# Optimization experiments

Hardware: AMD Instinct MI355X
Metric: run time of the kernel (lower is better)

The kernel has to match this reference:

```python
import jax, jax.numpy as jnp
import numpy as np

B, G, D = 256, 64, 20          # batch, genes per term, subsystem output dim
T3, T2, T1, T0 = 2048, 512, 128, 1  # terms per stratum, deepest first
FAN = 4                        # children per internal term (root gets all T1)
EPS = 1e-5                     # BatchNorm1d eps


def setup_inputs() -> dict:
    key = jax.random.key(0)
    ks = jax.random.split(key, 32)
    def genes(k, T):
        # binary gene perturbation states (column 3 of go_gene_strata_state)
        return (jax.random.uniform(k, (B, T, G)) < 0.5).astype(jnp.float32)
    def lin(kw, kb, T, din):
        # nn.init.uniform_(w, -0.001, 0.001) per DCellSubsystem
        W = jax.random.uniform(kw, (T, din, D), minval=-0.001, maxval=0.001)
        b = jax.random.uniform(kb, (T, D), minval=-0.001, maxval=0.001)
        return W, b
    in3, in2, in1, in0 = G, FAN * D + G, FAN * D + G, T1 * D + G
    W3, b3 = lin(ks[0], ks[1], T3, in3)
    W2, b2 = lin(ks[2], ks[3], T2, in2)
    W1, b1 = lin(ks[4], ks[5], T1, in1)
    W0, b0 = lin(ks[6], ks[7], T0, in0)
    ones = lambda T: jnp.ones((T, D), jnp.float32)
    zeros = lambda T: jnp.zeros((T, D), jnp.float32)
    hw0 = jax.random.normal(ks[8], (T0, D, 1)) * 0.1
    hb0 = jnp.zeros((T0, 1), jnp.float32)
    return {
        'genes3': genes(ks[9], T3), 'genes2': genes(ks[10], T2),
        'genes1': genes(ks[11], T1), 'genes0': genes(ks[12], T0),
        'W3': W3, 'b3': b3, 'g3': ones(T3), 'be3': zeros(T3),
        'W2': W2, 'b2': b2, 'g2': ones(T2), 'be2': zeros(T2),
        'W1': W1, 'b1': b1, 'g1': ones(T1), 'be1': zeros(T1),
        'W0': W0, 'b0': b0, 'g0': ones(T0), 'be0': zeros(T0),
        'hw0': hw0, 'hb0': hb0,
    }


def _subsystem(x, W, b, g, be):
    # Linear -> BatchNorm1d (training mode, batch stats over axis 0) -> Tanh
    z = jnp.einsum('bti,tio->bto', x, W) + b          # [B, T, D]
    mu = jnp.mean(z, axis=0)
    var = jnp.var(z, axis=0)                           # biased, as in torch BN
    zn = (z - mu) * jax.lax.rsqrt(var + EPS)
    return jnp.tanh(zn * g + be)


def reference(genes3, genes2, genes1, genes0,
              W3, b3, g3, be3, W2, b2, g2, be2,
              W1, b1, g1, be1, W0, b0, g0, be0, hw0, hb0):
    # stratum 3 (leaves): input is gene states only
    h3 = _subsystem(genes3, W3, b3, g3, be3)           # [B, T3, D]
    # stratum 2: concat FAN contiguous children + own gene states
    x2 = jnp.concatenate([h3.reshape(B, T2, FAN * D), genes2], axis=-1)
    h2 = _subsystem(x2, W2, b2, g2, be2)               # [B, T2, D]
    x1 = jnp.concatenate([h2.reshape(B, T1, FAN * D), genes1], axis=-1)
    h1 = _subsystem(x1, W1, b1, g1, be1)               # [B, T1, D]
    # root: all T1 children + root gene states
    x0 = jnp.concatenate([h1.reshape(B, T0, T1 * D), genes0], axis=-1)
    h0 = _subsystem(x0, W0, b0, g0, be0)               # [B, 1, D]
    pred = jnp.einsum('bto,toc->btc', h0, hw0) + hb0   # root linear head
    return pred.reshape(B, 1)
```

## Files before the change

### kernel.cpp

```cpp
#include <hip/hip_runtime.h>
#include <hip/hip_fp16.h>


#define DEV static __device__ __forceinline__

constexpr int B_  = 256, G_ = 64, D_ = 20;
constexpr int T3_ = 2048, T2_ = 512, T1_ = 128;
constexpr float EPS_ = 1e-5f;

typedef unsigned char u8;
typedef unsigned long long u64;

constexpr size_t OFF_GTB3 = 0;
constexpr size_t SZ_GTB3 = (size_t)T3_ * B_ * 8;
constexpr size_t OFF_GTB2 = OFF_GTB3 + SZ_GTB3;
constexpr size_t SZ_GTB2 = (size_t)T2_ * B_ * 8;
constexpr size_t OFF_GTB1 = OFF_GTB2 + SZ_GTB2;
constexpr size_t SZ_GTB1 = (size_t)T1_ * B_ * 8;
constexpr size_t OFF_H2B = OFF_GTB1 + SZ_GTB1;
constexpr size_t SZ_H2 = (size_t)T2_ * B_ * D_ * 2;
constexpr size_t OFF_H1B = OFF_H2B + SZ_H2;
constexpr size_t SZ_H1 = (size_t)T1_ * B_ * D_ * 2;
constexpr size_t OFF_Z0B = OFF_H1B + SZ_H1;

typedef _Float16 half8_t __attribute__((ext_vector_type(8)));
typedef float f32x4 __attribute__((ext_vector_type(4)));

DEV half8_t as_h8(uint4 u) {
    union { uint4 u4; half8_t h; } c; c.u4 = u; return c.h;
}

DEV half8_t bits8_to_h8(uint byte) {
    uint4 r;
    r.x = ((byte & 1u)        | ((byte & 2u)   << 15)) * 0x3C00u;
    r.y = (((byte >> 2) & 1u) | ((byte & 8u)   << 13)) * 0x3C00u;
    r.z = (((byte >> 4) & 1u) | ((byte & 32u)  << 11)) * 0x3C00u;
    r.w = (((byte >> 6) & 1u) | ((byte & 128u) << 9))  * 0x3C00u;
    return as_h8(r);
}

DEV float fast_tanh(float x) {
    float e = __expf(2.0f * x);
    return fmaf(-2.0f, __builtin_amdgcn_rcpf(e + 1.0f), 1.0f);
}

__global__ __launch_bounds__(256, 8) void k_pack_all(
        const float* __restrict__ g3s, const float* __restrict__ g2s,
        const float* __restrict__ g1s,
        u64* __restrict__ d3, u64* __restrict__ d2, u64* __restrict__ d1) {
    constexpr int R3 = B_ * T3_;
    constexpr int R2 = B_ * T2_;
    const int lane = threadIdx.x & 63;
    int R0 = (blockIdx.x * 4 + (threadIdx.x >> 6)) * 8;
    const float* src; u64* dst; int shift;
    if (R0 < R3)            { src = g3s; dst = d3; shift = 11; }
    else if (R0 < R3 + R2)  { R0 -= R3; src = g2s; dst = d2; shift = 9; }
    else                    { R0 -= R3 + R2; src = g1s; dst = d1; shift = 7; }

    const float* p = src + (size_t)R0 * G_ + lane;
    float x[8];
#pragma unroll
    for (int r = 0; r < 8; ++r) x[r] = p[r * G_];
    u64 m[8];
#pragma unroll
    for (int r = 0; r < 8; ++r) m[r] = __ballot(x[r] != 0.0f);

    if (lane < 8) {
        u64 v = m[0];
        v = lane == 1 ? m[1] : v;
        v = lane == 2 ? m[2] : v;
        v = lane == 3 ? m[3] : v;
        v = lane == 4 ? m[4] : v;
        v = lane == 5 ? m[5] : v;
        v = lane == 6 ? m[6] : v;
        v = lane == 7 ? m[7] : v;
        const int R = R0 + lane;
        const int b = R >> shift, t = R - (b << shift);
        dst[(size_t)t * B_ + b] = v;
    }
}

__global__ __launch_bounds__(256, 2) void k_gemm32(
        const u64* __restrict__ gTb3, const u64* __restrict__ gTb2,
        const float* __restrict__ W3, const float* __restrict__ g3,
        const float* __restrict__ be3,
        const float* __restrict__ W2, const float* __restrict__ g2,
        const float* __restrict__ be2, __half* __restrict__ h2out) {
    constexpr int STRB3 = 72, STRB2 = 200;
    __shared__ __align__(16) __half h3loc[4 * B_ * D_ + 16];
    __shared__ __align__(16) __half WT3[2][32 * STRB3];
    __shared__ __align__(16) __half WT2[32 * STRB2];
    __shared__ u64 gmask[5][B_];
    __shared__ float sredb[2][4][16], qredb[2][4][16];
    __shared__ float gv3[4 * D_], bev3[4 * D_], gv2[D_], bev2[D_];

    const int t = blockIdx.x, tid = threadIdx.x;
    const int w = tid >> 6, lane = tid & 63;

    u64 mreg[5];
#pragma unroll
    for (int c = 0; c < 4; ++c)
        mreg[c] = gTb3[(size_t)(4 * t + c) * B_ + tid];
    mreg[4] = gTb2[(size_t)t * B_ + tid];

    {
        uint* WTu = (uint*)WT2;
        for (int j = tid; j < 32 * STRB2 / 2; j += 256) WTu[j] = 0;
        if (tid < 16) h3loc[4 * B_ * D_ + tid] = __half(0.0f);
    }
#pragma unroll
    for (int s = 0; s < 5; ++s) gmask[s][tid] = mreg[s];
    __syncthreads();

    if (tid < 4 * D_) {
        gv3[tid] = g3[(size_t)(4 * t) * D_ + tid];
        bev3[tid] = be3[(size_t)(4 * t) * D_ + tid];
    } else if (tid < 5 * D_) {
        gv2[tid - 4 * D_] = g2[(size_t)t * D_ + (tid - 4 * D_)];
        bev2[tid - 4 * D_] = be2[(size_t)t * D_ + (tid - 4 * D_)];
    }
    {
        constexpr int NW2 = (144 * D_ + 255) / 256;
        const float* Wt = W2 + (size_t)t * (144 * D_);
        float wst[NW2];
#pragma unroll
        for (int i = 0; i < NW2; ++i) {
            int j = tid + i * 256;
            wst[i] = (j < 144 * D_) ? Wt[j] : 0.0f;
        }
        const float* W3t = W3 + (size_t)(4 * t) * (G_ * D_);
        float w3st[5];
#pragma unroll
        for (int i = 0; i < 5; ++i) w3st[i] = W3t[tid + i * 256];
#pragma unroll
        for (int i = 0; i < NW2; ++i) {
            int j = tid + i * 256;
            if (j < 144 * D_) {
                int k_orig = j / D_, o = j - k_orig * D_;
                int k_lds;
                if (k_orig < 4 * D_) {
                    int c = k_orig / D_;
                    k_lds = c * 32 + (k_orig - c * D_);
                } else {
                    k_lds = 4 * 32 + (k_orig - 4 * D_);
                }
                WT2[o * STRB2 + k_lds] = __float2half(wst[i]);
            }
        }
#pragma unroll
        for (int i = 0; i < 5; ++i) {
            int j = tid + i * 256;
            int k = j / D_, o = j - k * D_;
            WT3[0][o * STRB3 + k] = __float2half(w3st[i]);
        }
    }
    __syncthreads();

    const int quad = lane >> 4, l15 = lane & 15;
    const int nt = w >> 1, mhalf = w & 1;
    const int ocol = nt * 16 + l15;
    const int brow_base = mhalf * 128;
    const int shq = quad * 8;
    const int oc = ocol < D_ ? ocol : D_ - 1;

#pragma unroll
    for (int c = 0; c < 4; ++c) {
        float wreg[5];
        if (c < 3) {
            const float* W3n = W3 + (size_t)(4 * t + c + 1) * (G_ * D_);
#pragma unroll
            for (int i = 0; i < 5; ++i) wreg[i] = W3n[tid + i * 256];
        }
        const __half* WTc = WT3[c & 1];
        half8_t Bf0 = as_h8(*(const uint4*)(WTc + ocol * STRB3 + quad * 8));
        half8_t Bf1 = as_h8(*(const uint4*)(WTc + ocol * STRB3 + 32 + quad * 8));

        f32x4 acc[8];
#pragma unroll
        for (int mt = 0; mt < 8; ++mt) acc[mt] = (f32x4){0.f, 0.f, 0.f, 0.f};
#pragma unroll
        for (int mt = 0; mt < 8; ++mt) {
            const int bA = brow_base + mt * 16 + l15;
            const u64 gm = gmask[c][bA];
            acc[mt] = __builtin_amdgcn_mfma_f32_16x16x32_f16(
                bits8_to_h8(((uint)gm >> shq) & 0xFFu), Bf0, acc[mt], 0, 0, 0);
            acc[mt] = __builtin_amdgcn_mfma_f32_16x16x32_f16(
                bits8_to_h8(((uint)(gm >> 32) >> shq) & 0xFFu), Bf1, acc[mt], 0, 0, 0);
        }

        if (c < 3) {
#pragma unroll
            for (int i = 0; i < 5; ++i) {
                int j = tid + i * 256;
                int k = j / D_, o = j - k * D_;
                WT3[(c + 1) & 1][o * STRB3 + k] = __float2half(wreg[i]);
            }
        }

        float s = 0.f, q = 0.f;
#pragma unroll
        for (int mt = 0; mt < 8; ++mt)
#pragma unroll
            for (int r = 0; r < 4; ++r) {
                float z = acc[mt][r];
                s += z; q += z * z;
            }
        s += __shfl_xor(s, 16, 64); q += __shfl_xor(q, 16, 64);
        s += __shfl_xor(s, 32, 64); q += __shfl_xor(q, 32, 64);
        if (lane < 16) { sredb[c & 1][w][lane] = s; qredb[c & 1][w][lane] = q; }
        __syncthreads();
        const float S = sredb[c & 1][2 * nt][l15] + sredb[c & 1][2 * nt + 1][l15];
        const float Q = qredb[c & 1][2 * nt][l15] + qredb[c & 1][2 * nt + 1][l15];
        const float mu  = S * (1.0f / B_);
        const float var = fmaxf(Q * (1.0f / B_) - mu * mu, 0.0f);
        const float rstd = rsqrtf(var + EPS_);
        const float A = rstd * gv3[c * D_ + oc];
        const float C = bev3[c * D_ + oc] - mu * A;
        if (ocol < D_) {
#pragma unroll
            for (int mt = 0; mt < 8; ++mt)
#pragma unroll
                for (int r = 0; r < 4; ++r) {
                    float h = fast_tanh(fmaf(A, acc[mt][r], C));
                    int b = brow_base + mt * 16 + quad * 4 + r;
                    h3loc[(size_t)(c * B_ + b) * D_ + ocol] = __float2half(h);
                }
        }
    }
    __syncthreads();

    half8_t Bf[6];
#pragma unroll
    for (int ks = 0; ks < 6; ++ks)
        Bf[ks] = as_h8(*(const uint4*)(WT2 + ocol * STRB2 + ks * 32 + quad * 8));

    f32x4 acc[8];
#pragma unroll
    for (int mt = 0; mt < 8; ++mt) acc[mt] = (f32x4){0.f, 0.f, 0.f, 0.f};
#pragma unroll
    for (int mt = 0; mt < 8; ++mt) {
        const int bA = brow_base + mt * 16 + l15;
        const u64 gm = gmask[4][bA];
#pragma unroll
        for (int c = 0; c < 4; ++c) {
            const __half* ap = h3loc + (size_t)(c * B_ + bA) * D_ + quad * 8;
            uint2 u0 = *(const uint2*)(ap);
            uint2 u1 = *(const uint2*)(ap + 4);
            acc[mt] = __builtin_amdgcn_mfma_f32_16x16x32_f16(
                as_h8(make_uint4(u0.x, u0.y, u1.x, u1.y)), Bf[c], acc[mt], 0, 0, 0);
        }
        acc[mt] = __builtin_amdgcn_mfma_f32_16x16x32_f16(
            bits8_to_h8(((uint)gm >> shq) & 0xFFu), Bf[4], acc[mt], 0, 0, 0);
        acc[mt] = __builtin_amdgcn_mfma_f32_16x16x32_f16(
            bits8_to_h8(((uint)(gm >> 32) >> shq) & 0xFFu), Bf[5], acc[mt], 0, 0, 0);
    }

    float s = 0.f, q = 0.f;
#pragma unroll
    for (int mt = 0; mt < 8; ++mt)
#pragma unroll
        for (int r = 0; r < 4; ++r) {
            float z = acc[mt][r];
            s += z; q += z * z;
        }
    s += __shfl_xor(s, 16, 64); q += __shfl_xor(q, 16, 64);
    s += __shfl_xor(s, 32, 64); q += __shfl_xor(q, 32, 64);
    if (lane < 16) { sredb[0][w][lane] = s; qredb[0][w][lane] = q; }
    __syncthreads();
    const float S = sredb[0][2 * nt][l15] + sredb[0][2 * nt + 1][l15];
    const float Q = qredb[0][2 * nt][l15] + qredb[0][2 * nt + 1][l15];
    const float mu  = S * (1.0f / B_);
    const float var = fmaxf(Q * (1.0f / B_) - mu * mu, 0.0f);
    const float rstd = rsqrtf(var + EPS_);
    const float A = rstd * gv2[oc];
    const float C = bev2[oc] - mu * A;

    __half* ebuf = WT2;
    if (ocol < D_) {
#pragma unroll
        for (int mt = 0; mt < 8; ++mt)
#pragma unroll
            for (int r = 0; r < 4; ++r) {
                float h = fast_tanh(fmaf(A, acc[mt][r], C));
                int b = brow_base + mt * 16 + quad * 4 + r;
                ebuf[b * D_ + ocol] = __float2half(h);
            }
    }
    __syncthreads();
    const uint4* src4 = (const uint4*)ebuf;
    uint4* dst4 = (uint4*)(h2out + (size_t)t * (B_ * D_));
    for (int j = tid; j < (B_ * D_) / 8; j += 256) dst4[j] = src4[j];
}

template <int T, int NCHILD>
__global__ __launch_bounds__(256, 4) void k_gemm(const __half* __restrict__ hsrc,
                                                 const u64* __restrict__ gTb,
                                                 const float* __restrict__ W,
                                                 const float* __restrict__ g,
                                                 const float* __restrict__ be,
                                                 __half* __restrict__ hout) {
    constexpr int K_IN = NCHILD * 20 + 64;
    constexpr int NK = NCHILD + 2;
    constexpr int STRB = NCHILD ? 200 : 72;
    constexpr int LDSH = (32 * STRB > B_ * D_) ? 32 * STRB : B_ * D_;
    __shared__ __align__(16) __half WT[LDSH];
    __shared__ float gv[D_], bev[D_];
    __shared__ float sred[4][16], qred[4][16];
    __shared__ u64 gmask[B_];

    const int t = blockIdx.x, tid = threadIdx.x;
    const int w = tid >> 6, lane = tid & 63;

    const u64 mreg = gTb[(size_t)t * B_ + tid];

    if (NCHILD) {
        uint* WTu = (uint*)WT;
        for (int j = tid; j < 32 * STRB / 2; j += 256) WTu[j] = 0;
    }
    gmask[tid] = mreg;
    __syncthreads();

    if (tid < D_) { gv[tid] = g[t * D_ + tid]; bev[tid] = be[t * D_ + tid]; }
    {
        constexpr int NST = (K_IN * D_ + 255) / 256;
        const float* Wt = W + (size_t)t * (K_IN * D_);
        float wst[NST];
#pragma unroll
        for (int i = 0; i < NST; ++i) {
            int j = tid + i * 256;
            wst[i] = (j < K_IN * D_) ? Wt[j] : 0.0f;
        }
#pragma unroll
        for (int i = 0; i < NST; ++i) {
            int j = tid + i * 256;
            if (j < K_IN * D_) {
                int k_orig = j / D_, o = j - k_orig * D_;
                int k_lds;
                if (NCHILD && k_orig < NCHILD * D_) {
                    int c = k_orig / D_;
                    k_lds = c * 32 + (k_orig - c * D_);
                } else {
                    k_lds = NCHILD * 32 + (k_orig - NCHILD * D_);
                }
                WT[o * STRB + k_lds] = __float2half(wst[i]);
            }
        }
    }
    __syncthreads();

    const int quad = lane >> 4, l15 = lane & 15;
    const int nt = w >> 1, mhalf = w & 1;
    const int ocol = nt * 16 + l15;
    const int brow_base = mhalf * 128;
    const int shq = quad * 8;

    half8_t Bf[NK];
#pragma unroll
    for (int ks = 0; ks < NK; ++ks)
        Bf[ks] = as_h8(*(const uint4*)(WT + ocol * STRB + ks * 32 + quad * 8));

    f32x4 acc[8];
#pragma unroll
    for (int mt = 0; mt < 8; ++mt) acc[mt] = (f32x4){0.f, 0.f, 0.f, 0.f};

#pragma unroll
    for (int mt = 0; mt < 8; ++mt) {
        const int bA = brow_base + mt * 16 + l15;
        const u64 gm = gmask[bA];
#pragma unroll
        for (int c = 0; c < NCHILD; ++c) {
            const __half* ap = hsrc + ((size_t)(NCHILD * t + c) * B_ + bA) * D_ + quad * 8;
            uint2 u0 = *(const uint2*)(ap);
            uint2 u1 = *(const uint2*)(ap + 4);
            acc[mt] = __builtin_amdgcn_mfma_f32_16x16x32_f16(
                as_h8(make_uint4(u0.x, u0.y, u1.x, u1.y)), Bf[c], acc[mt], 0, 0, 0);
        }
        acc[mt] = __builtin_amdgcn_mfma_f32_16x16x32_f16(
            bits8_to_h8(((uint)gm >> shq) & 0xFFu), Bf[NCHILD], acc[mt], 0, 0, 0);
        acc[mt] = __builtin_amdgcn_mfma_f32_16x16x32_f16(
            bits8_to_h8(((uint)(gm >> 32) >> shq) & 0xFFu), Bf[NCHILD + 1], acc[mt], 0, 0, 0);
    }

    float s = 0.f, q = 0.f;
#pragma unroll
    for (int mt = 0; mt < 8; ++mt)
#pragma unroll
        for (int r = 0; r < 4; ++r) {
            float z = acc[mt][r];
            s += z; q += z * z;
        }
    s += __shfl_xor(s, 16, 64); q += __shfl_xor(q, 16, 64);
    s += __shfl_xor(s, 32, 64); q += __shfl_xor(q, 32, 64);
    if (lane < 16) { sred[w][lane] = s; qred[w][lane] = q; }
    __syncthreads();
    const float S = sred[2 * nt][l15] + sred[2 * nt + 1][l15];
    const float Q = qred[2 * nt][l15] + qred[2 * nt + 1][l15];
    const float mu  = S * (1.0f / B_);
    const float var = fmaxf(Q * (1.0f / B_) - mu * mu, 0.0f);
    const float rstd = rsqrtf(var + EPS_);
    const int oc = ocol < D_ ? ocol : D_ - 1;
    const float A = rstd * gv[oc];
    const float C = bev[oc] - mu * A;

    if (ocol < D_) {
#pragma unroll
        for (int mt = 0; mt < 8; ++mt)
#pragma unroll
            for (int r = 0; r < 4; ++r) {
                float h = fast_tanh(fmaf(A, acc[mt][r], C));
                int b = brow_base + mt * 16 + quad * 4 + r;
                WT[b * D_ + ocol] = __float2half(h);
            }
    }
    __syncthreads();
    const uint4* src4 = (const uint4*)WT;
    uint4* dst4 = (uint4*)(hout + (size_t)t * (B_ * D_));
    for (int j = tid; j < (B_ * D_) / 8; j += 256) dst4[j] = src4[j];
}

__global__ __launch_bounds__(256, 4) void k_stage0a(const __half* __restrict__ h1,
                                                    const float* __restrict__ genes0,
                                                    const float* __restrict__ W0,
                                                    float* __restrict__ z0p) {
    const int b = blockIdx.x >> 2, s = blockIdx.x & 3, tid = threadIdx.x;
    const int kbase = 640 * s;
    float acc[D_] = {};
#pragma unroll
    for (int j = 0; j < 3; ++j) {
        int kl = tid + 256 * j;
        if (kl < 640) {
            int k = kbase + kl;
            int tt = k / D_, o = k - tt * D_;
            float xk = __half2float(h1[((size_t)tt * B_ + b) * D_ + o]);
            const float4* w = (const float4*)(W0 + (size_t)k * D_);
#pragma unroll
            for (int v = 0; v < D_ / 4; ++v) {
                float4 f = w[v];
                acc[4 * v + 0] = fmaf(xk, f.x, acc[4 * v + 0]);
                acc[4 * v + 1] = fmaf(xk, f.y, acc[4 * v + 1]);
                acc[4 * v + 2] = fmaf(xk, f.z, acc[4 * v + 2]);
                acc[4 * v + 3] = fmaf(xk, f.w, acc[4 * v + 3]);
            }
        }
    }
    if (s == 3 && tid < G_) {
        float xk = genes0[(size_t)b * G_ + tid];
        const float4* w = (const float4*)(W0 + (size_t)(T1_ * D_ + tid) * D_);
#pragma unroll
        for (int v = 0; v < D_ / 4; ++v) {
            float4 f = w[v];
            acc[4 * v + 0] = fmaf(xk, f.x, acc[4 * v + 0]);
            acc[4 * v + 1] = fmaf(xk, f.y, acc[4 * v + 1]);
            acc[4 * v + 2] = fmaf(xk, f.z, acc[4 * v + 2]);
            acc[4 * v + 3] = fmaf(xk, f.w, acc[4 * v + 3]);
        }
    }
    __shared__ float sred[4][D_];
    const int lane = tid & 63, wave = tid >> 6;
#pragma unroll
    for (int off = 32; off; off >>= 1)
#pragma unroll
        for (int o = 0; o < D_; ++o) acc[o] += __shfl_xor(acc[o], off, 64);
    if (lane == 0)
#pragma unroll
        for (int o = 0; o < D_; ++o) sred[wave][o] = acc[o];
    __syncthreads();
    if (tid < D_)
        z0p[((size_t)b * 4 + s) * D_ + tid] =
            sred[0][tid] + sred[1][tid] + sred[2][tid] + sred[3][tid];
}

__global__ __launch_bounds__(256) void k_stage0b(const float* __restrict__ z0p,
                                                 const float* __restrict__ g0,
                                                 const float* __restrict__ be0,
                                                 const float* __restrict__ hw0,
                                                 const float* __restrict__ hb0,
                                                 float* __restrict__ out) {
    const int tid = threadIdx.x;
    float acc[D_] = {};
#pragma unroll
    for (int s = 0; s < 4; ++s) {
        const float4* zp = (const float4*)(z0p + ((size_t)tid * 4 + s) * D_);
#pragma unroll
        for (int v = 0; v < D_ / 4; ++v) {
            float4 f = zp[v];
            acc[4 * v + 0] += f.x; acc[4 * v + 1] += f.y;
            acc[4 * v + 2] += f.z; acc[4 * v + 3] += f.w;
        }
    }
    __shared__ float sred[4][D_], qred[4][D_], Avec[D_], Cvec[D_], hwv[D_ + 1];
    const int lane = tid & 63, wave = tid >> 6;
    float s[D_], q[D_];
#pragma unroll
    for (int o = 0; o < D_; ++o) { s[o] = acc[o]; q[o] = acc[o] * acc[o]; }
#pragma unroll
    for (int off = 32; off; off >>= 1) {
#pragma unroll
        for (int o = 0; o < D_; ++o) {
            s[o] += __shfl_xor(s[o], off, 64);
            q[o] += __shfl_xor(q[o], off, 64);
        }
    }
    if (lane == 0) {
#pragma unroll
        for (int o = 0; o < D_; ++o) { sred[wave][o] = s[o]; qred[wave][o] = q[o]; }
    }
    __syncthreads();
    if (tid < D_) {
        float S = sred[0][tid] + sred[1][tid] + sred[2][tid] + sred[3][tid];
        float Q = qred[0][tid] + qred[1][tid] + qred[2][tid] + qred[3][tid];
        float mu  = S * (1.0f / B_);
        float var = fmaxf(Q * (1.0f / B_) - mu * mu, 0.0f);
        float rstd = rsqrtf(var + EPS_);
        float A = rstd * g0[tid];
        Avec[tid] = A;
        Cvec[tid] = be0[tid] - mu * A;
        hwv[tid] = hw0[tid];
    }
    if (tid == 0) hwv[D_] = hb0[0];
    __syncthreads();
    float pred = hwv[D_];
#pragma unroll
    for (int o = 0; o < D_; ++o) {
        float h = fast_tanh(fmaf(acc[o], Avec[o], Cvec[o]));
        pred = fmaf(h, hwv[o], pred);
    }
    out[tid] = pred;
}

extern "C" void kernel_launch(void* const* d_in, const int* in_sizes, int n_in,
                              void* d_out, int out_size, void* d_ws, size_t ws_size,
                              hipStream_t stream) {
    const float* genes3 = (const float*)d_in[0];
    const float* genes2 = (const float*)d_in[1];
    const float* genes1 = (const float*)d_in[2];
    const float* genes0 = (const float*)d_in[3];
    const float* W3  = (const float*)d_in[4];
    const float* g3  = (const float*)d_in[6];
    const float* be3 = (const float*)d_in[7];
    const float* W2  = (const float*)d_in[8];
    const float* g2  = (const float*)d_in[10];
    const float* be2 = (const float*)d_in[11];
    const float* W1  = (const float*)d_in[12];
    const float* g1  = (const float*)d_in[14];
    const float* be1 = (const float*)d_in[15];
    const float* W0  = (const float*)d_in[16];
    const float* g0  = (const float*)d_in[18];
    const float* be0 = (const float*)d_in[19];
    const float* hw0 = (const float*)d_in[20];
    const float* hb0 = (const float*)d_in[21];

    char* wsb = (char*)d_ws;
    u64* gTb3 = (u64*)(wsb + OFF_GTB3);
    u64* gTb2 = (u64*)(wsb + OFF_GTB2);
    u64* gTb1 = (u64*)(wsb + OFF_GTB1);
    __half* h2  = (__half*)(wsb + OFF_H2B);
    __half* h1  = (__half*)(wsb + OFF_H1B);
    float*  z0p = (float*)(wsb + OFF_Z0B);

    k_pack_all<<<688128 / 32, 256, 0, stream>>>(genes3, genes2, genes1,
                                                gTb3, gTb2, gTb1);
    k_gemm32<<<T2_, 256, 0, stream>>>(gTb3, gTb2, W3, g3, be3,
                                      W2, g2, be2, h2);
    k_gemm<T1_, 4><<<T1_, 256, 0, stream>>>(h2, gTb1, W1, g1, be1, h1);
    k_stage0a<<<B_ * 4, 256, 0, stream>>>(h1, genes0, W0, z0p);
    k_stage0b<<<1, 256, 0, stream>>>(z0p, g0, be0, hw0, hb0, (float*)d_out);
}
```

Baseline: 305.1 us.

## Fuse gene bit-packing into stratum-3/2 GEMM via cooperative grid sync

```diff
diff --git a/kernel.cpp b/kernel.cpp
--- a/kernel.cpp
+++ b/kernel.cpp
@@ -1,6 +1,9 @@
 #include <hip/hip_runtime.h>
 #include <hip/hip_fp16.h>
-
+#include <hip/hip_cooperative_groups.h>
+
+
+namespace cg = cooperative_groups;
 
 #define DEV static __device__ __forceinline__
 
@@ -44,44 +47,10 @@
     return fmaf(-2.0f, __builtin_amdgcn_rcpf(e + 1.0f), 1.0f);
 }
 
-__global__ __launch_bounds__(256, 8) void k_pack_all(
-        const float* __restrict__ g3s, const float* __restrict__ g2s,
-        const float* __restrict__ g1s,
-        u64* __restrict__ d3, u64* __restrict__ d2, u64* __restrict__ d1) {
-    constexpr int R3 = B_ * T3_;
-    constexpr int R2 = B_ * T2_;
-    const int lane = threadIdx.x & 63;
-    int R0 = (blockIdx.x * 4 + (threadIdx.x >> 6)) * 8;
-    const float* src; u64* dst; int shift;
-    if (R0 < R3)            { src = g3s; dst = d3; shift = 11; }
-    else if (R0 < R3 + R2)  { R0 -= R3; src = g2s; dst = d2; shift = 9; }
-    else                    { R0 -= R3 + R2; src = g1s; dst = d1; shift = 7; }
-
-    const float* p = src + (size_t)R0 * G_ + lane;
-    float x[8];
-#pragma unroll
-    for (int r = 0; r < 8; ++r) x[r] = p[r * G_];
-    u64 m[8];
-#pragma unroll
-    for (int r = 0; r < 8; ++r) m[r] = __ballot(x[r] != 0.0f);
-
-    if (lane < 8) {
-        u64 v = m[0];
-        v = lane == 1 ? m[1] : v;
-        v = lane == 2 ? m[2] : v;
-        v = lane == 3 ? m[3] : v;
-        v = lane == 4 ? m[4] : v;
-        v = lane == 5 ? m[5] : v;
-        v = lane == 6 ? m[6] : v;
-        v = lane == 7 ? m[7] : v;
-        const int R = R0 + lane;
-        const int b = R >> shift, t = R - (b << shift);
-        dst[(size_t)t * B_ + b] = v;
-    }
-}
-
-__global__ __launch_bounds__(256, 2) void k_gemm32(
-        const u64* __restrict__ gTb3, const u64* __restrict__ gTb2,
+__global__ __launch_bounds__(256, 2) void k_packgemm32(
+        const float* __restrict__ genes3f, const float* __restrict__ genes2f,
+        const float* __restrict__ genes1f,
+        u64* __restrict__ gTb3, u64* __restrict__ gTb2, u64* __restrict__ gTb1,
         const float* __restrict__ W3, const float* __restrict__ g3,
         const float* __restrict__ be3,
         const float* __restrict__ W2, const float* __restrict__ g2,
@@ -96,6 +65,36 @@
 
     const int t = blockIdx.x, tid = threadIdx.x;
     const int w = tid >> 6, lane = tid & 63;
+
+    {
+        const int gwave = blockIdx.x * 4 + w;
+        constexpr int R3 = B_ * T3_;
+        constexpr int R2 = B_ * T2_;
+#pragma unroll 2
+        for (int it = 0; it < 21; ++it) {
+            int R0 = (gwave + it * 2048) * 16;
+            const float* src; u64* dst; int shift; int Rb;
+            if (R0 < R3)           { src = genes3f; dst = gTb3; shift = 11; Rb = R0; }
+            else if (R0 < R3 + R2) { src = genes2f; dst = gTb2; shift = 9;  Rb = R0 - R3; }
+            else                   { src = genes1f; dst = gTb1; shift = 7;  Rb = R0 - R3 - R2; }
+            const float* p = src + (size_t)Rb * G_ + lane;
+            float x[16];
+#pragma unroll
+            for (int r = 0; r < 16; ++r) x[r] = p[(size_t)r * G_];
+            u64 m = 0;
+#pragma unroll
+            for (int r = 0; r < 16; ++r) {
+                u64 mm = __ballot(x[r] != 0.0f);
+                if (lane == r) m = mm;
+            }
+            if (lane < 16) {
+                const int R = Rb + lane;
+                const int b = R >> shift, tt = R - (b << shift);
+                dst[(size_t)tt * B_ + b] = m;
+            }
+        }
+    }
+    cg::this_grid().sync();
 
     u64 mreg[5];
 #pragma unroll
@@ -558,10 +557,14 @@
     __half* h1  = (__half*)(wsb + OFF_H1B);
     float*  z0p = (float*)(wsb + OFF_Z0B);
 
-    k_pack_all<<<688128 / 32, 256, 0, stream>>>(genes3, genes2, genes1,
-                                                gTb3, gTb2, gTb1);
-    k_gemm32<<<T2_, 256, 0, stream>>>(gTb3, gTb2, W3, g3, be3,
-                                      W2, g2, be2, h2);
+    void* kargs[] = {
+        (void*)&genes3, (void*)&genes2, (void*)&genes1,
+        (void*)&gTb3, (void*)&gTb2, (void*)&gTb1,
+        (void*)&W3, (void*)&g3, (void*)&be3,
+        (void*)&W2, (void*)&g2, (void*)&be2,
+        (void*)&h2};
+    hipLaunchCooperativeKernel((void*)k_packgemm32, dim3(T2_), dim3(256),
+                               kargs, 0, stream);
     k_gemm<T1_, 4><<<T1_, 256, 0, stream>>>(h2, gTb1, W1, g1, be1, h1);
     k_stage0a<<<B_ * 4, 256, 0, stream>>>(h1, genes0, W0, z0p);
     k_stage0b<<<1, 256, 0, stream>>>(z0p, g0, be0, hw0, hb0, (float*)d_out);
```

Result: slower. 419.5 us (+37.5%).

## Assign one stratum-3 child term per wave to remove per-child block syncs

Applied to the files above, without the earlier changes.

```diff
diff --git a/kernel.cpp b/kernel.cpp
--- a/kernel.cpp
+++ b/kernel.cpp
@@ -88,29 +88,29 @@
         const float* __restrict__ be2, __half* __restrict__ h2out) {
     constexpr int STRB3 = 72, STRB2 = 200;
     __shared__ __align__(16) __half h3loc[4 * B_ * D_ + 16];
-    __shared__ __align__(16) __half WT3[2][32 * STRB3];
+    __shared__ __align__(16) __half WT3[4][32 * STRB3];
     __shared__ __align__(16) __half WT2[32 * STRB2];
-    __shared__ u64 gmask[5][B_];
-    __shared__ float sredb[2][4][16], qredb[2][4][16];
+    __shared__ u64 gmask2[B_];
+    __shared__ float sred2[4][16], qred2[4][16];
     __shared__ float gv3[4 * D_], bev3[4 * D_], gv2[D_], bev2[D_];
 
     const int t = blockIdx.x, tid = threadIdx.x;
     const int w = tid >> 6, lane = tid & 63;
-
-    u64 mreg[5];
-#pragma unroll
-    for (int c = 0; c < 4; ++c)
-        mreg[c] = gTb3[(size_t)(4 * t + c) * B_ + tid];
-    mreg[4] = gTb2[(size_t)t * B_ + tid];
+    const int quad = lane >> 4, l15 = lane & 15;
+    const int shq = quad * 8;
+
+    u64 gm[16];
+#pragma unroll
+    for (int mt = 0; mt < 16; ++mt)
+        gm[mt] = gTb3[(size_t)(4 * t + w) * B_ + mt * 16 + l15];
+    const u64 m2 = gTb2[(size_t)t * B_ + tid];
 
     {
         uint* WTu = (uint*)WT2;
         for (int j = tid; j < 32 * STRB2 / 2; j += 256) WTu[j] = 0;
         if (tid < 16) h3loc[4 * B_ * D_ + tid] = __half(0.0f);
     }
-#pragma unroll
-    for (int s = 0; s < 5; ++s) gmask[s][tid] = mreg[s];
-    __syncthreads();
+    gmask2[tid] = m2;
 
     if (tid < 4 * D_) {
         gv3[tid] = g3[(size_t)(4 * t) * D_ + tid];
@@ -119,7 +119,12 @@
         gv2[tid - 4 * D_] = g2[(size_t)t * D_ + (tid - 4 * D_)];
         bev2[tid - 4 * D_] = be2[(size_t)t * D_ + (tid - 4 * D_)];
     }
+
     {
+        const float* W3t = W3 + (size_t)(4 * t) * (G_ * D_);
+        float w3st[20];
+#pragma unroll
+        for (int i = 0; i < 20; ++i) w3st[i] = W3t[tid + i * 256];
         constexpr int NW2 = (144 * D_ + 255) / 256;
         const float* Wt = W2 + (size_t)t * (144 * D_);
         float wst[NW2];
@@ -128,10 +133,14 @@
             int j = tid + i * 256;
             wst[i] = (j < 144 * D_) ? Wt[j] : 0.0f;
         }
-        const float* W3t = W3 + (size_t)(4 * t) * (G_ * D_);
-        float w3st[5];
-#pragma unroll
-        for (int i = 0; i < 5; ++i) w3st[i] = W3t[tid + i * 256];
+#pragma unroll
+        for (int i = 0; i < 20; ++i) {
+            int j = tid + i * 256;
+            int c = j / (G_ * D_);
+            int jj = j - c * (G_ * D_);
+            int k = jj / D_, o = jj - k * D_;
+            WT3[c][o * STRB3 + k] = __float2half(w3st[i]);
+        }
 #pragma unroll
         for (int i = 0; i < NW2; ++i) {
             int j = tid + i * 256;
@@ -147,87 +156,76 @@
                 WT2[o * STRB2 + k_lds] = __float2half(wst[i]);
             }
         }
-#pragma unroll
-        for (int i = 0; i < 5; ++i) {
-            int j = tid + i * 256;
-            int k = j / D_, o = j - k * D_;
-            WT3[0][o * STRB3 + k] = __float2half(w3st[i]);
-        }
-    }
-    __syncthreads();
-
-    const int quad = lane >> 4, l15 = lane & 15;
+    }
+    __syncthreads();
+
+    {
+        const __half* WTc = WT3[w];
+        half8_t Bf3[2][2];
+#pragma unroll
+        for (int nt = 0; nt < 2; ++nt)
+#pragma unroll
+            for (int ks = 0; ks < 2; ++ks)
+                Bf3[nt][ks] = as_h8(*(const uint4*)(
+                    WTc + (nt * 16 + l15) * STRB3 + ks * 32 + quad * 8));
+
+        f32x4 acc3[16][2];
+#pragma unroll
+        for (int mt = 0; mt < 16; ++mt)
+#pragma unroll
+            for (int nt = 0; nt < 2; ++nt)
+                acc3[mt][nt] = (f32x4){0.f, 0.f, 0.f, 0.f};
+
+#pragma unroll
+        for (int mt = 0; mt < 16; ++mt) {
+            half8_t a0 = bits8_to_h8(((uint)gm[mt] >> shq) & 0xFFu);
+            half8_t a1 = bits8_to_h8(((uint)(gm[mt] >> 32) >> shq) & 0xFFu);
+#pragma unroll
+            for (int nt = 0; nt < 2; ++nt) {
+                acc3[mt][nt] = __builtin_amdgcn_mfma_f32_16x16x32_f16(
+                    a0, Bf3[nt][0], acc3[mt][nt], 0, 0, 0);
+                acc3[mt][nt] = __builtin_amdgcn_mfma_f32_16x16x32_f16(
+                    a1, Bf3[nt][1], acc3[mt][nt], 0, 0, 0);
+            }
+        }
+
+#pragma unroll
+        for (int nt = 0; nt < 2; ++nt) {
+            float s = 0.f, q = 0.f;
+#pragma unroll
+            for (int mt = 0; mt < 16; ++mt)
+#pragma unroll
+                for (int r = 0; r < 4; ++r) {
+                    float z = acc3[mt][nt][r];
+                    s += z; q += z * z;
+                }
+            s += __shfl_xor(s, 16, 64); q += __shfl_xor(q, 16, 64);
+            s += __shfl_xor(s, 32, 64); q += __shfl_xor(q, 32, 64);
+            const int col = nt * 16 + l15;
+            const int oc = col < D_ ? col : D_ - 1;
+            const float mu  = s * (1.0f / B_);
+            const float var = fmaxf(q * (1.0f / B_) - mu * mu, 0.0f);
+            const float rstd = rsqrtf(var + EPS_);
+            const float A = rstd * gv3[w * D_ + oc];
+            const float C = bev3[w * D_ + oc] - mu * A;
+            if (col < D_) {
+#pragma unroll
+                for (int mt = 0; mt < 16; ++mt)
+#pragma unroll
+                    for (int r = 0; r < 4; ++r) {
+                        float h = fast_tanh(fmaf(A, acc3[mt][nt][r], C));
+                        int row = mt * 16 + quad * 4 + r;
+                        h3loc[(size_t)(w * B_ + row) * D_ + col] = __float2half(h);
+                    }
+            }
+        }
+    }
+    __syncthreads();
+
     const int nt = w >> 1, mhalf = w & 1;
     const int ocol = nt * 16 + l15;
     const int brow_base = mhalf * 128;
-    const int shq = quad * 8;
     const int oc = ocol < D_ ? ocol : D_ - 1;
-
-#pragma unroll
-    for (int c = 0; c < 4; ++c) {
-        float wreg[5];
-        if (c < 3) {
-            const float* W3n = W3 + (size_t)(4 * t + c + 1) * (G_ * D_);
-#pragma unroll
-            for (int i = 0; i < 5; ++i) wreg[i] = W3n[tid + i * 256];
-        }
-        const __half* WTc = WT3[c & 1];
-        half8_t Bf0 = as_h8(*(const uint4*)(WTc + ocol * STRB3 + quad * 8));
-        half8_t Bf1 = as_h8(*(const uint4*)(WTc + ocol * STRB3 + 32 + quad * 8));
-
-        f32x4 acc[8];
-#pragma unroll
-        for (int mt = 0; mt < 8; ++mt) acc[mt] = (f32x4){0.f, 0.f, 0.f, 0.f};
-#pragma unroll
-        for (int mt = 0; mt < 8; ++mt) {
-            const int bA = brow_base + mt * 16 + l15;
-            const u64 gm = gmask[c][bA];
-            acc[mt] = __builtin_amdgcn_mfma_f32_16x16x32_f16(
-                bits8_to_h8(((uint)gm >> shq) & 0xFFu), Bf0, acc[mt], 0, 0, 0);
-            acc[mt] = __builtin_amdgcn_mfma_f32_16x16x32_f16(
-                bits8_to_h8(((uint)(gm >> 32) >> shq) & 0xFFu), Bf1, acc[mt], 0, 0, 0);
-        }
-
-        if (c < 3) {
-#pragma unroll
-            for (int i = 0; i < 5; ++i) {
-                int j = tid + i * 256;
-                int k = j / D_, o = j - k * D_;
-                WT3[(c + 1) & 1][o * STRB3 + k] = __float2half(wreg[i]);
-            }
-        }
-
-        float s = 0.f, q = 0.f;
-#pragma unroll
-        for (int mt = 0; mt < 8; ++mt)
-#pragma unroll
-            for (int r = 0; r < 4; ++r) {
-                float z = acc[mt][r];
-                s += z; q += z * z;
-            }
-        s += __shfl_xor(s, 16, 64); q += __shfl_xor(q, 16, 64);
-        s += __shfl_xor(s, 32, 64); q += __shfl_xor(q, 32, 64);
-        if (lane < 16) { sredb[c & 1][w][lane] = s; qredb[c & 1][w][lane] = q; }
-        __syncthreads();
-        const float S = sredb[c & 1][2 * nt][l15] + sredb[c & 1][2 * nt + 1][l15];
-        const float Q = qredb[c & 1][2 * nt][l15] + qredb[c & 1][2 * nt + 1][l15];
-        const float mu  = S * (1.0f / B_);
-        const float var = fmaxf(Q * (1.0f / B_) - mu * mu, 0.0f);
-        const float rstd = rsqrtf(var + EPS_);
-        const float A = rstd * gv3[c * D_ + oc];
-        const float C = bev3[c * D_ + oc] - mu * A;
-        if (ocol < D_) {
-#pragma unroll
-            for (int mt = 0; mt < 8; ++mt)
-#pragma unroll
-                for (int r = 0; r < 4; ++r) {
-                    float h = fast_tanh(fmaf(A, acc[mt][r], C));
-                    int b = brow_base + mt * 16 + quad * 4 + r;
-                    h3loc[(size_t)(c * B_ + b) * D_ + ocol] = __float2half(h);
-                }
-        }
-    }
-    __syncthreads();
 
     half8_t Bf[6];
 #pragma unroll
@@ -240,7 +238,7 @@
 #pragma unroll
     for (int mt = 0; mt < 8; ++mt) {
         const int bA = brow_base + mt * 16 + l15;
-        const u64 gm = gmask[4][bA];
+        const u64 g2m = gmask2[bA];
 #pragma unroll
         for (int c = 0; c < 4; ++c) {
             const __half* ap = h3loc + (size_t)(c * B_ + bA) * D_ + quad * 8;
@@ -250,9 +248,9 @@
                 as_h8(make_uint4(u0.x, u0.y, u1.x, u1.y)), Bf[c], acc[mt], 0, 0, 0);
         }
         acc[mt] = __builtin_amdgcn_mfma_f32_16x16x32_f16(
-            bits8_to_h8(((uint)gm >> shq) & 0xFFu), Bf[4], acc[mt], 0, 0, 0);
+            bits8_to_h8(((uint)g2m >> shq) & 0xFFu), Bf[4], acc[mt], 0, 0, 0);
         acc[mt] = __builtin_amdgcn_mfma_f32_16x16x32_f16(
-            bits8_to_h8(((uint)(gm >> 32) >> shq) & 0xFFu), Bf[5], acc[mt], 0, 0, 0);
+            bits8_to_h8(((uint)(g2m >> 32) >> shq) & 0xFFu), Bf[5], acc[mt], 0, 0, 0);
     }
 
     float s = 0.f, q = 0.f;
@@ -265,10 +263,10 @@
         }
     s += __shfl_xor(s, 16, 64); q += __shfl_xor(q, 16, 64);
     s += __shfl_xor(s, 32, 64); q += __shfl_xor(q, 32, 64);
-    if (lane < 16) { sredb[0][w][lane] = s; qredb[0][w][lane] = q; }
-    __syncthreads();
-    const float S = sredb[0][2 * nt][l15] + sredb[0][2 * nt + 1][l15];
-    const float Q = qredb[0][2 * nt][l15] + qredb[0][2 * nt + 1][l15];
+    if (lane < 16) { sred2[w][lane] = s; qred2[w][lane] = q; }
+    __syncthreads();
+    const float S = sred2[2 * nt][l15] + sred2[2 * nt + 1][l15];
+    const float Q = qred2[2 * nt][l15] + qred2[2 * nt + 1][l15];
     const float mu  = S * (1.0f / B_);
     const float var = fmaxf(Q * (1.0f / B_) - mu * mu, 0.0f);
     const float rstd = rsqrtf(var + EPS_);
```

New measurement: 305.1 us. Within noise of the previous version (-0.0%).
